# Kernel tuning notes

Hardware: AMD Instinct MI355X
Metric: run time of the kernel (lower is better)

The kernel has to match this reference:

```python
import jax, jax.numpy as jnp
import numpy as np

WIN = 3  # win_size from init


def setup_inputs() -> dict:
    key = jax.random.key(0)
    ks = jax.random.split(key, 7)
    B, H, W, d = 8, 128, 128, 128
    N = H * W
    s = d ** -0.5  # param init scale
    return {
        "x": jax.random.normal(ks[0], (B, N, d), dtype=jnp.float32),
        "Wq": jax.random.normal(ks[1], (d, d), dtype=jnp.float32) * s,
        "bq": jax.random.normal(ks[2], (d,), dtype=jnp.float32) * 0.01,
        "Wk": jax.random.normal(ks[3], (d, d), dtype=jnp.float32) * s,
        "bk": jax.random.normal(ks[4], (d,), dtype=jnp.float32) * 0.01,
        "Wv": jax.random.normal(ks[5], (d, d), dtype=jnp.float32) * s,
        "bv": jax.random.normal(ks[6], (d,), dtype=jnp.float32) * 0.01,
        "H": H,
        "W": W,
    }


def reference(x, Wq, bq, Wk, bk, Wv, bv, H, W):
    B, N, d = x.shape
    scale = d ** -0.5
    pad = WIN // 2

    q = (x @ Wq + bq).reshape(B, H, W, d)
    k = (x @ Wk + bk).reshape(B, H, W, d)
    v = (x @ Wv + bv).reshape(B, H, W, d)

    # zero-pad spatial dims (matches F.pad); padded neighbors get logit 0, not -inf
    k_pad = jnp.pad(k, ((0, 0), (pad, pad), (pad, pad), (0, 0)))
    v_pad = jnp.pad(v, ((0, 0), (pad, pad), (pad, pad), (0, 0)))

    scores_l, vs_l = [], []
    for dy in range(WIN):
        for dx in range(WIN):
            k_slice = k_pad[:, dy:dy + H, dx:dx + W]   # [B,H,W,d]
            v_slice = v_pad[:, dy:dy + H, dx:dx + W]
            scores_l.append(jnp.einsum("bhwd,bhwd->bhw", q, k_slice) * scale)
            vs_l.append(v_slice)

    scores = jnp.stack(scores_l, axis=-1)            # [B,H,W,9]
    prob = jax.nn.softmax(scores, axis=-1)           # [B,H,W,9]
    v_stk = jnp.stack(vs_l, axis=-1)                 # [B,H,W,d,9]
    out = jnp.einsum("bhwn,bhwdn->bhwd", prob, v_stk)
    return out.reshape(B, N, d)
```

## Files before the change

kernel.cpp:

```cpp
#include <hip/hip_runtime.h>
#include <stdint.h>

#define B_ 8
#define H_ 128
#define W_ 128
#define D_ 128
#define N_ (H_*W_)
#define M_ (B_*N_)

typedef __attribute__((ext_vector_type(8))) short short8;
typedef __attribute__((ext_vector_type(4))) float floatx4;

typedef const __attribute__((address_space(1))) void* gas_t;
typedef __attribute__((address_space(3))) void* las_t;

__device__ inline unsigned short f2bf(float f){
  union { float f; unsigned int i; } c; c.f = f;
  unsigned int x = c.i;
  x += 0x7FFF + ((x >> 16) & 1);
  return (unsigned short)(x >> 16);
}
__device__ inline float bflo(unsigned int u){
  union { unsigned int i; float f; } c; c.i = u << 16; return c.f;
}
__device__ inline float bfhi(unsigned int u){
  union { unsigned int i; float f; } c; c.i = u & 0xFFFF0000u; return c.f;
}

__global__ void wtrans_kernel(const float* __restrict__ Wq, const float* __restrict__ Wk,
                              const float* __restrict__ Wv, unsigned short* __restrict__ Wt){
  const float* src = blockIdx.x == 0 ? Wq : (blockIdx.x == 1 ? Wk : Wv);
  unsigned short* dst = Wt + blockIdx.x * (D_*D_);
  const int i = blockIdx.y * 256 + threadIdx.x;
  const int k = i >> 7, n = i & 127;
  dst[n*D_ + k] = f2bf(src[i]);
}

__global__ __launch_bounds__(256, 2) void qkv_gemm_kernel(
    const float* __restrict__ x, const unsigned short* __restrict__ Wt,
    const float* __restrict__ bq, const float* __restrict__ bk, const float* __restrict__ bv,
    unsigned short* __restrict__ Q, unsigned short* __restrict__ K, unsigned short* __restrict__ V)
{
  const int rowTile = blockIdx.x;

  __shared__ unsigned short lds[32768];

  const int t = threadIdx.x;
  const int wave = t >> 6, lane = t & 63;

  {
    const float* xrow = x + (size_t)rowTile * 128 * D_;
    #pragma unroll
    for (int p = 0; p < 8; ++p){
      int s = p*256 + t;
      int r = s >> 4, cp = s & 15, c = cp ^ (r & 7);
      const float* gp = xrow + r*D_ + c*8;
      float4 f0 = *(const float4*)gp;
      float4 f1 = *(const float4*)(gp + 4);
      uint4 pk;
      pk.x = (unsigned)f2bf(f0.x) | ((unsigned)f2bf(f0.y) << 16);
      pk.y = (unsigned)f2bf(f0.z) | ((unsigned)f2bf(f0.w) << 16);
      pk.z = (unsigned)f2bf(f1.x) | ((unsigned)f2bf(f1.y) << 16);
      pk.w = (unsigned)f2bf(f1.z) | ((unsigned)f2bf(f1.w) << 16);
      *(uint4*)&lds[s*8] = pk;
    }
  }

  const int wm = (wave >> 1) * 64, wn = (wave & 1) * 64;
  const int m0 = lane & 15, quad = lane >> 4;

  #pragma unroll
  for (int which = 0; which < 3; ++which){
    const float* bias = which == 0 ? bq : (which == 1 ? bk : bv);
    unsigned short* Out = which == 0 ? Q : (which == 1 ? K : V);
    const unsigned short* Wsel = Wt + which * (D_*D_);

    #pragma unroll
    for (int p = 0; p < 8; ++p){
      int s = p*256 + t;
      int n = s >> 4, cp = s & 15, c = cp ^ (n & 7);
      const unsigned short* gp = Wsel + n*128 + c*8;
      unsigned short* lp = (unsigned short*)lds + 16384 + p*2048 + wave*512;
      __builtin_amdgcn_global_load_lds((gas_t)(const void*)gp, (las_t)(void*)lp, 16, 0, 0);
    }
    __syncthreads();

    floatx4 acc[4][4] = {};
    #pragma unroll
    for (int kk = 0; kk < 4; ++kk){
      short8 a[4], b[4];
      #pragma unroll
      for (int i = 0; i < 4; ++i){
        int row = wm + i*16 + m0;
        int c = (kk*4 + quad) ^ (row & 7);
        a[i] = *(const short8*)&lds[row*128 + c*8];
      }
      #pragma unroll
      for (int j = 0; j < 4; ++j){
        int n = wn + j*16 + m0;
        int c = (kk*4 + quad) ^ (n & 7);
        b[j] = *(const short8*)&lds[16384 + n*128 + c*8];
      }
      #pragma unroll
      for (int i = 0; i < 4; ++i)
        #pragma unroll
        for (int j = 0; j < 4; ++j)
          acc[i][j] = __builtin_amdgcn_mfma_f32_16x16x32_bf16(a[i], b[j], acc[i][j], 0, 0, 0);
    }

    __syncthreads();
    unsigned short* Outp = Out + (size_t)rowTile * 128 * D_;
    #pragma unroll
    for (int half = 0; half < 2; ++half){
      if ((wave >> 1) == half){
        #pragma unroll
        for (int j = 0; j < 4; ++j){
          const int col = wn + j*16 + m0;
          const float bb = bias[col];
          #pragma unroll
          for (int i = 0; i < 4; ++i){
            #pragma unroll
            for (int r = 0; r < 4; ++r){
              int lrow = i*16 + quad*4 + r;
              lds[16384 + lrow*136 + col] = f2bf(acc[i][j][r] + bb);
            }
          }
        }
      }
      __syncthreads();
      #pragma unroll
      for (int p = 0; p < 4; ++p){
        int rr = p*16 + (t >> 4), cc = t & 15;
        uint4 vv = *(const uint4*)&lds[16384 + rr*136 + cc*8];
        *(uint4*)(Outp + half*8192 + p*2048 + t*8) = vv;
      }
      __syncthreads();
    }
  }
}

__global__ __launch_bounds__(256, 2) void attn_kernel(
    const unsigned short* __restrict__ Q, const unsigned short* __restrict__ K,
    const unsigned short* __restrict__ V, float* __restrict__ out)
{
  const int t = threadIdx.x;
  const int e8 = t & 7;
  const int pix = blockIdx.x * 32 + (t >> 3);
  const int w = pix & 127;
  const int h = (pix >> 7) & 127;
  const int bbase = pix & ~(N_ - 1);
  const float scale = 0.08838834764831845f;
  const int doff = e8 * 16;
  const size_t off = (size_t)pix * D_ + doff;

  int npix[9]; bool okm[9];
  #pragma unroll
  for (int i = 0; i < 9; ++i){
    const int dy = i/3 - 1, dx = i%3 - 1;
    const int hh = h + dy, ww = w + dx;
    okm[i] = ((unsigned)hh < 128u) && ((unsigned)ww < 128u);
    const int hc = min(max(hh, 0), 127);
    const int wc = min(max(ww, 0), 127);
    npix[i] = bbase + hc*W_ + wc;
  }

  uint4 qu0, qu1;
  {
    const unsigned short* qp = Q + off;
    qu0 = *(const uint4*)qp;
    qu1 = *(const uint4*)(qp + 8);
  }
  uint4 ku[9][2];
  #pragma unroll
  for (int i = 0; i < 9; ++i){
    const unsigned short* kp = K + (size_t)npix[i]*D_ + doff;
    ku[i][0] = *(const uint4*)kp;
    ku[i][1] = *(const uint4*)(kp + 8);
  }
  uint4 vu[9][2];
  #pragma unroll
  for (int i = 0; i < 9; ++i){
    const unsigned short* vp = V + (size_t)npix[i]*D_ + doff;
    vu[i][0] = *(const uint4*)vp;
    vu[i][1] = *(const uint4*)(vp + 8);
  }

  float q[16];
  {
    unsigned uu[8] = {qu0.x, qu0.y, qu0.z, qu0.w, qu1.x, qu1.y, qu1.z, qu1.w};
    #pragma unroll
    for (int e = 0; e < 8; ++e){
      q[e*2]     = bflo(uu[e]) * scale;
      q[e*2 + 1] = bfhi(uu[e]) * scale;
    }
  }

  float s[9];
  #pragma unroll
  for (int i = 0; i < 9; ++i){
    unsigned uu[8] = {ku[i][0].x, ku[i][0].y, ku[i][0].z, ku[i][0].w,
                      ku[i][1].x, ku[i][1].y, ku[i][1].z, ku[i][1].w};
    float acc = 0.f;
    #pragma unroll
    for (int e = 0; e < 8; ++e){
      acc += q[e*2]     * bflo(uu[e]);
      acc += q[e*2 + 1] * bfhi(uu[e]);
    }
    s[i] = okm[i] ? acc : 0.f;
  }
  #pragma unroll
  for (int i = 0; i < 9; ++i){
    s[i] += __shfl_xor(s[i], 1, 64);
    s[i] += __shfl_xor(s[i], 2, 64);
    s[i] += __shfl_xor(s[i], 4, 64);
  }

  float m = s[0];
  #pragma unroll
  for (int i = 1; i < 9; ++i) m = fmaxf(m, s[i]);
  float p[9]; float l = 0.f;
  #pragma unroll
  for (int i = 0; i < 9; ++i){ p[i] = __expf(s[i] - m); l += p[i]; }
  const float inv = 1.f / l;

  float o[16];
  #pragma unroll
  for (int d = 0; d < 16; ++d) o[d] = 0.f;
  #pragma unroll
  for (int i = 0; i < 9; ++i){
    const float pi = okm[i] ? p[i] * inv : 0.f;
    unsigned uu[8] = {vu[i][0].x, vu[i][0].y, vu[i][0].z, vu[i][0].w,
                      vu[i][1].x, vu[i][1].y, vu[i][1].z, vu[i][1].w};
    #pragma unroll
    for (int e = 0; e < 8; ++e){
      o[e*2]     += pi * bflo(uu[e]);
      o[e*2 + 1] += pi * bfhi(uu[e]);
    }
  }

  float* op = out + off;
  #pragma unroll
  for (int c = 0; c < 4; ++c){
    float4 v4 = make_float4(o[c*4], o[c*4+1], o[c*4+2], o[c*4+3]);
    *(float4*)(op + c*4) = v4;
  }
}

extern "C" void kernel_launch(void* const* d_in, const int* in_sizes, int n_in,
                              void* d_out, int out_size, void* d_ws, size_t ws_size,
                              hipStream_t stream)
{
  const float* x  = (const float*)d_in[0];
  const float* Wq = (const float*)d_in[1];
  const float* bq = (const float*)d_in[2];
  const float* Wk = (const float*)d_in[3];
  const float* bk = (const float*)d_in[4];
  const float* Wv = (const float*)d_in[5];
  const float* bv = (const float*)d_in[6];
  float* out = (float*)d_out;

  char* ws = (char*)d_ws;
  unsigned short* Wt = (unsigned short*)ws;
  unsigned short* Q  = (unsigned short*)(ws + (1<<17));
  unsigned short* K  = (unsigned short*)(ws + (1<<17) + (size_t)M_*D_*2);
  unsigned short* V  = (unsigned short*)(ws + (1<<17) + (size_t)2*M_*D_*2);

  hipLaunchKernelGGL(wtrans_kernel, dim3(3, 64), dim3(256), 0, stream, Wq, Wk, Wv, Wt);
  hipLaunchKernelGGL(qkv_gemm_kernel, dim3(M_/128), dim3(256), 0, stream,
                     x, Wt, bq, bk, bv, Q, K, V);
  hipLaunchKernelGGL(attn_kernel, dim3(M_/32), dim3(256), 0, stream, Q, K, V, out);
}
```

Before: 194.9 us.

## Halve QKV GEMM row tile, store from registers, prefetch next weight

The QKV projection kernel now processes 64 rows per block instead of 128. This cuts LDS to 48KB, doubles the grid and raises launch bounds to 3 blocks per CU for higher occupancy. The MFMA operands are swapped so each lane holds row-contiguous output, and results are written straight to global memory as packed bf16 pairs instead of being staged through LDS, which removes several barriers. The next weight matrix is loaded into LDS while the current results are being stored. In exchange, each block reloads the weights for only half as many rows, and the direct stores are narrower, less coalesced writes.

Result: slower. 201.5 us (+3.4%).

```diff
diff --git a/kernel.cpp b/kernel.cpp
--- a/kernel.cpp
+++ b/kernel.cpp
@@ -36,22 +36,34 @@
   dst[n*D_ + k] = f2bf(src[i]);
 }
 
-__global__ __launch_bounds__(256, 2) void qkv_gemm_kernel(
+__global__ __launch_bounds__(256, 3) void qkv_gemm_kernel(
     const float* __restrict__ x, const unsigned short* __restrict__ Wt,
     const float* __restrict__ bq, const float* __restrict__ bk, const float* __restrict__ bv,
     unsigned short* __restrict__ Q, unsigned short* __restrict__ K, unsigned short* __restrict__ V)
 {
   const int rowTile = blockIdx.x;
 
-  __shared__ unsigned short lds[32768];
+  __shared__ unsigned short lds[24576];
 
   const int t = threadIdx.x;
   const int wave = t >> 6, lane = t & 63;
 
   {
-    const float* xrow = x + (size_t)rowTile * 128 * D_;
+    const unsigned short* W0 = Wt;
     #pragma unroll
     for (int p = 0; p < 8; ++p){
+      int s = p*256 + t;
+      int n = s >> 4, cp = s & 15, c = cp ^ (n & 7);
+      const unsigned short* gp = W0 + n*128 + c*8;
+      unsigned short* lp = (unsigned short*)lds + 8192 + p*2048 + wave*512;
+      __builtin_amdgcn_global_load_lds((gas_t)(const void*)gp, (las_t)(void*)lp, 16, 0, 0);
+    }
+  }
+
+  {
+    const float* xrow = x + (size_t)rowTile * 64 * D_;
+    #pragma unroll
+    for (int p = 0; p < 4; ++p){
       int s = p*256 + t;
       int r = s >> 4, cp = s & 15, c = cp ^ (r & 7);
       const float* gp = xrow + r*D_ + c*8;
@@ -65,32 +77,19 @@
       *(uint4*)&lds[s*8] = pk;
     }
   }
-
-  const int wm = (wave >> 1) * 64, wn = (wave & 1) * 64;
+  __syncthreads();
+
+  const int wm = (wave >> 1) * 32, wn = (wave & 1) * 64;
   const int m0 = lane & 15, quad = lane >> 4;
 
   #pragma unroll
   for (int which = 0; which < 3; ++which){
-    const float* bias = which == 0 ? bq : (which == 1 ? bk : bv);
-    unsigned short* Out = which == 0 ? Q : (which == 1 ? K : V);
-    const unsigned short* Wsel = Wt + which * (D_*D_);
-
-    #pragma unroll
-    for (int p = 0; p < 8; ++p){
-      int s = p*256 + t;
-      int n = s >> 4, cp = s & 15, c = cp ^ (n & 7);
-      const unsigned short* gp = Wsel + n*128 + c*8;
-      unsigned short* lp = (unsigned short*)lds + 16384 + p*2048 + wave*512;
-      __builtin_amdgcn_global_load_lds((gas_t)(const void*)gp, (las_t)(void*)lp, 16, 0, 0);
-    }
-    __syncthreads();
-
-    floatx4 acc[4][4] = {};
+    floatx4 acc[4][2] = {};
     #pragma unroll
     for (int kk = 0; kk < 4; ++kk){
-      short8 a[4], b[4];
-      #pragma unroll
-      for (int i = 0; i < 4; ++i){
+      short8 a[2], b[4];
+      #pragma unroll
+      for (int i = 0; i < 2; ++i){
         int row = wm + i*16 + m0;
         int c = (kk*4 + quad) ^ (row & 7);
         a[i] = *(const short8*)&lds[row*128 + c*8];
@@ -99,43 +98,47 @@
       for (int j = 0; j < 4; ++j){
         int n = wn + j*16 + m0;
         int c = (kk*4 + quad) ^ (n & 7);
-        b[j] = *(const short8*)&lds[16384 + n*128 + c*8];
-      }
-      #pragma unroll
-      for (int i = 0; i < 4; ++i)
+        b[j] = *(const short8*)&lds[8192 + n*128 + c*8];
+      }
+      #pragma unroll
+      for (int j = 0; j < 4; ++j)
         #pragma unroll
-        for (int j = 0; j < 4; ++j)
-          acc[i][j] = __builtin_amdgcn_mfma_f32_16x16x32_bf16(a[i], b[j], acc[i][j], 0, 0, 0);
-    }
-
+        for (int i = 0; i < 2; ++i)
+          acc[j][i] = __builtin_amdgcn_mfma_f32_16x16x32_bf16(b[j], a[i], acc[j][i], 0, 0, 0);
+    }
     __syncthreads();
-    unsigned short* Outp = Out + (size_t)rowTile * 128 * D_;
-    #pragma unroll
-    for (int half = 0; half < 2; ++half){
-      if ((wave >> 1) == half){
+
+    if (which < 2){
+      const unsigned short* Wnext = Wt + (which + 1) * (D_*D_);
+      #pragma unroll
+      for (int p = 0; p < 8; ++p){
+        int s = p*256 + t;
+        int n = s >> 4, cp = s & 15, c = cp ^ (n & 7);
+        const unsigned short* gp = Wnext + n*128 + c*8;
+        unsigned short* lp = (unsigned short*)lds + 8192 + p*2048 + wave*512;
+        __builtin_amdgcn_global_load_lds((gas_t)(const void*)gp, (las_t)(void*)lp, 16, 0, 0);
+      }
+    }
+
+    {
+      const float* bias = which == 0 ? bq : (which == 1 ? bk : bv);
+      unsigned short* Out = which == 0 ? Q : (which == 1 ? K : V);
+      unsigned short* Outp = Out + (size_t)rowTile * 64 * D_;
+      #pragma unroll
+      for (int j = 0; j < 4; ++j){
+        const float4 bb = *(const float4*)&bias[wn + j*16 + quad*4];
         #pragma unroll
-        for (int j = 0; j < 4; ++j){
-          const int col = wn + j*16 + m0;
-          const float bb = bias[col];
-          #pragma unroll
-          for (int i = 0; i < 4; ++i){
-            #pragma unroll
-            for (int r = 0; r < 4; ++r){
-              int lrow = i*16 + quad*4 + r;
-              lds[16384 + lrow*136 + col] = f2bf(acc[i][j][r] + bb);
-            }
-          }
+        for (int i = 0; i < 2; ++i){
+          const int row = wm + i*16 + m0;
+          uint2 pk;
+          pk.x = (unsigned)f2bf(acc[j][i][0] + bb.x) | ((unsigned)f2bf(acc[j][i][1] + bb.y) << 16);
+          pk.y = (unsigned)f2bf(acc[j][i][2] + bb.z) | ((unsigned)f2bf(acc[j][i][3] + bb.w) << 16);
+          *(uint2*)(Outp + row*D_ + wn + j*16 + quad*4) = pk;
         }
       }
-      __syncthreads();
-      #pragma unroll
-      for (int p = 0; p < 4; ++p){
-        int rr = p*16 + (t >> 4), cc = t & 15;
-        uint4 vv = *(const uint4*)&lds[16384 + rr*136 + cc*8];
-        *(uint4*)(Outp + half*8192 + p*2048 + t*8) = vv;
-      }
-      __syncthreads();
-    }
+    }
+
+    if (which < 2) __syncthreads();
   }
 }
 
@@ -266,7 +269,7 @@
   unsigned short* V  = (unsigned short*)(ws + (1<<17) + (size_t)2*M_*D_*2);
 
   hipLaunchKernelGGL(wtrans_kernel, dim3(3, 64), dim3(256), 0, stream, Wq, Wk, Wv, Wt);
-  hipLaunchKernelGGL(qkv_gemm_kernel, dim3(M_/128), dim3(256), 0, stream,
+  hipLaunchKernelGGL(qkv_gemm_kernel, dim3(M_/64), dim3(256), 0, stream,
                      x, Wt, bq, bk, bv, Q, K, V);
   hipLaunchKernelGGL(attn_kernel, dim3(M_/32), dim3(256), 0, stream, Q, K, V, out);
 }
```

## Keep x fragments in registers and store GEMM output directly from MFMA accumulators

Applied to the files above, without the earlier changes.

The QKV GEMM now loads each wave's x rows straight from global memory into register-resident bf16 MFMA A-fragments once, instead of staging them in LDS and re-reading them for every weight matrix. Operands are swapped so the accumulator layout yields four contiguous output columns per lane, which are written to global memory directly without an LDS transpose and the extra barriers it needed. LDS use is halved to hold only the weight tile, which may improve occupancy. The cost is more registers for the held fragments and narrower 8-byte global stores.

Result: slower. 202.6 us (+4.0%).

```diff
diff --git a/kernel.cpp b/kernel.cpp
--- a/kernel.cpp
+++ b/kernel.cpp
@@ -43,96 +43,102 @@
 {
   const int rowTile = blockIdx.x;
 
-  __shared__ unsigned short lds[32768];
+  __shared__ unsigned short lds[16384];
 
   const int t = threadIdx.x;
   const int wave = t >> 6, lane = t & 63;
+  const int m0 = lane & 15, quad = lane >> 4;
+  const int wm = (wave >> 1) * 64, wn = (wave & 1) * 64;
 
   {
-    const float* xrow = x + (size_t)rowTile * 128 * D_;
-    #pragma unroll
-    for (int p = 0; p < 8; ++p){
-      int s = p*256 + t;
-      int r = s >> 4, cp = s & 15, c = cp ^ (r & 7);
-      const float* gp = xrow + r*D_ + c*8;
-      float4 f0 = *(const float4*)gp;
-      float4 f1 = *(const float4*)(gp + 4);
-      uint4 pk;
-      pk.x = (unsigned)f2bf(f0.x) | ((unsigned)f2bf(f0.y) << 16);
-      pk.y = (unsigned)f2bf(f0.z) | ((unsigned)f2bf(f0.w) << 16);
-      pk.z = (unsigned)f2bf(f1.x) | ((unsigned)f2bf(f1.y) << 16);
-      pk.w = (unsigned)f2bf(f1.z) | ((unsigned)f2bf(f1.w) << 16);
-      *(uint4*)&lds[s*8] = pk;
-    }
-  }
-
-  const int wm = (wave >> 1) * 64, wn = (wave & 1) * 64;
-  const int m0 = lane & 15, quad = lane >> 4;
-
-  #pragma unroll
-  for (int which = 0; which < 3; ++which){
-    const float* bias = which == 0 ? bq : (which == 1 ? bk : bv);
-    unsigned short* Out = which == 0 ? Q : (which == 1 ? K : V);
-    const unsigned short* Wsel = Wt + which * (D_*D_);
-
     #pragma unroll
     for (int p = 0; p < 8; ++p){
       int s = p*256 + t;
       int n = s >> 4, cp = s & 15, c = cp ^ (n & 7);
-      const unsigned short* gp = Wsel + n*128 + c*8;
-      unsigned short* lp = (unsigned short*)lds + 16384 + p*2048 + wave*512;
-      __builtin_amdgcn_global_load_lds((gas_t)(const void*)gp, (las_t)(void*)lp, 16, 0, 0);
-    }
-    __syncthreads();
-
+      __builtin_amdgcn_global_load_lds((gas_t)(const void*)(Wt + n*128 + c*8),
+                                       (las_t)(void*)((unsigned short*)lds + p*2048 + wave*512),
+                                       16, 0, 0);
+    }
+  }
+
+  short8 a[4][4];
+  const float* xbase = x + (size_t)(rowTile*128 + wm + m0) * D_ + quad*8;
+  #pragma unroll
+  for (int half = 0; half < 2; ++half){
+    float4 f[8][2];
+    #pragma unroll
+    for (int kk2 = 0; kk2 < 2; ++kk2)
+      #pragma unroll
+      for (int i = 0; i < 4; ++i){
+        const float* gp = xbase + i*16*D_ + (half*2 + kk2)*32;
+        f[kk2*4+i][0] = *(const float4*)gp;
+        f[kk2*4+i][1] = *(const float4*)(gp + 4);
+      }
+    #pragma unroll
+    for (int kk2 = 0; kk2 < 2; ++kk2)
+      #pragma unroll
+      for (int i = 0; i < 4; ++i){
+        short8 v;
+        v[0] = (short)f2bf(f[kk2*4+i][0].x);
+        v[1] = (short)f2bf(f[kk2*4+i][0].y);
+        v[2] = (short)f2bf(f[kk2*4+i][0].z);
+        v[3] = (short)f2bf(f[kk2*4+i][0].w);
+        v[4] = (short)f2bf(f[kk2*4+i][1].x);
+        v[5] = (short)f2bf(f[kk2*4+i][1].y);
+        v[6] = (short)f2bf(f[kk2*4+i][1].z);
+        v[7] = (short)f2bf(f[kk2*4+i][1].w);
+        a[half*2 + kk2][i] = v;
+      }
+  }
+  __syncthreads();
+
+  #pragma unroll
+  for (int which = 0; which < 3; ++which){
     floatx4 acc[4][4] = {};
     #pragma unroll
     for (int kk = 0; kk < 4; ++kk){
-      short8 a[4], b[4];
-      #pragma unroll
-      for (int i = 0; i < 4; ++i){
-        int row = wm + i*16 + m0;
-        int c = (kk*4 + quad) ^ (row & 7);
-        a[i] = *(const short8*)&lds[row*128 + c*8];
-      }
+      short8 b[4];
       #pragma unroll
       for (int j = 0; j < 4; ++j){
         int n = wn + j*16 + m0;
         int c = (kk*4 + quad) ^ (n & 7);
-        b[j] = *(const short8*)&lds[16384 + n*128 + c*8];
-      }
-      #pragma unroll
-      for (int i = 0; i < 4; ++i)
+        b[j] = *(const short8*)&lds[n*128 + c*8];
+      }
+      #pragma unroll
+      for (int j = 0; j < 4; ++j)
         #pragma unroll
-        for (int j = 0; j < 4; ++j)
-          acc[i][j] = __builtin_amdgcn_mfma_f32_16x16x32_bf16(a[i], b[j], acc[i][j], 0, 0, 0);
-    }
-
-    __syncthreads();
-    unsigned short* Outp = Out + (size_t)rowTile * 128 * D_;
-    #pragma unroll
-    for (int half = 0; half < 2; ++half){
-      if ((wave >> 1) == half){
+        for (int i = 0; i < 4; ++i)
+          acc[j][i] = __builtin_amdgcn_mfma_f32_16x16x32_bf16(b[j], a[kk][i], acc[j][i], 0, 0, 0);
+    }
+
+    {
+      const float* bias = which == 0 ? bq : (which == 1 ? bk : bv);
+      unsigned short* Out = which == 0 ? Q : (which == 1 ? K : V);
+      unsigned short* Outp = Out + (size_t)rowTile * 128 * D_;
+      #pragma unroll
+      for (int j = 0; j < 4; ++j){
+        const float4 bb = *(const float4*)&bias[wn + j*16 + quad*4];
         #pragma unroll
-        for (int j = 0; j < 4; ++j){
-          const int col = wn + j*16 + m0;
-          const float bb = bias[col];
-          #pragma unroll
-          for (int i = 0; i < 4; ++i){
-            #pragma unroll
-            for (int r = 0; r < 4; ++r){
-              int lrow = i*16 + quad*4 + r;
-              lds[16384 + lrow*136 + col] = f2bf(acc[i][j][r] + bb);
-            }
-          }
+        for (int i = 0; i < 4; ++i){
+          const int row = wm + i*16 + m0;
+          uint2 pk;
+          pk.x = (unsigned)f2bf(acc[j][i][0] + bb.x) | ((unsigned)f2bf(acc[j][i][1] + bb.y) << 16);
+          pk.y = (unsigned)f2bf(acc[j][i][2] + bb.z) | ((unsigned)f2bf(acc[j][i][3] + bb.w) << 16);
+          *(uint2*)(Outp + row*D_ + wn + j*16 + quad*4) = pk;
         }
       }
+    }
+
+    if (which < 2){
       __syncthreads();
-      #pragma unroll
-      for (int p = 0; p < 4; ++p){
-        int rr = p*16 + (t >> 4), cc = t & 15;
-        uint4 vv = *(const uint4*)&lds[16384 + rr*136 + cc*8];
-        *(uint4*)(Outp + half*8192 + p*2048 + t*8) = vv;
+      const unsigned short* Wnext = Wt + (which + 1) * (D_*D_);
+      #pragma unroll
+      for (int p = 0; p < 8; ++p){
+        int s = p*256 + t;
+        int n = s >> 4, cp = s & 15, c = cp ^ (n & 7);
+        __builtin_amdgcn_global_load_lds((gas_t)(const void*)(Wnext + n*128 + c*8),
+                                         (las_t)(void*)((unsigned short*)lds + p*2048 + wave*512),
+                                         16, 0, 0);
       }
       __syncthreads();
     }
```
